# Kernel optimization log

Measured on AMD Instinct MI355X. Metric: run time of the kernel, lower is better.

Reference implementation:

```python
import jax, jax.numpy as jnp
import numpy as np

V, SMAX, D, H, L, DFF, W = 32000, 1024, 1024, 16, 2, 4096, 256
HD = D // H
EPS = 1e-6


def setup_inputs() -> dict:
    key = jax.random.key(0)
    ks = jax.random.split(key, 20)
    s = lambda k, shape, scale=0.02: jax.random.normal(k, shape, dtype=jnp.float32) * scale
    return {
        "input_ids": jax.random.randint(ks[0], (2, SMAX), 0, V, dtype=jnp.int64),
        "emb": s(ks[1], (V, D)),
        "pos": s(ks[2], (SMAX, D)),
        "norm1_w": jnp.ones((L, D), jnp.float32),
        "norm2_w": jnp.ones((L, D), jnp.float32),
        "wq": s(ks[3], (L, D, D)), "bq": jnp.zeros((L, D), jnp.float32),
        "wk": s(ks[4], (L, D, D)), "bk": jnp.zeros((L, D), jnp.float32),
        "wv": s(ks[5], (L, D, D)), "bv": jnp.zeros((L, D), jnp.float32),
        "wo": s(ks[6], (L, D, D)), "bo": jnp.zeros((L, D), jnp.float32),
        "w1": s(ks[7], (L, D, DFF)), "b1": jnp.zeros((L, DFF), jnp.float32),
        "w2": s(ks[8], (L, DFF, D)), "b2": jnp.zeros((L, D), jnp.float32),
        "normf_w": jnp.ones((D,), jnp.float32),
    }


def rms(x, w):
    return x * jax.lax.rsqrt(jnp.mean(x * x, axis=-1, keepdims=True) + EPS) * w


def reference(input_ids, emb, pos, norm1_w, norm2_w, wq, bq, wk, bk, wv, bv,
              wo, bo, w1, b1, w2, b2, normf_w):
    B, S = input_ids.shape
    x = emb[input_ids] + pos[:S]  # [B,S,D]
    # sliding-window causal mask: attend to j with 0 <= i-j < W
    i = jnp.arange(S)[:, None]
    j = jnp.arange(S)[None, :]
    mask = (j <= i) & (i - j < W)  # [S,S]
    neg = jnp.asarray(-1e9, x.dtype)
    for l in range(L):
        h = rms(x, norm1_w[l])
        q = (h @ wq[l] + bq[l]).reshape(B, S, H, HD)
        k = (h @ wk[l] + bk[l]).reshape(B, S, H, HD)
        v = (h @ wv[l] + bv[l]).reshape(B, S, H, HD)
        scores = jnp.einsum('bqhd,bkhd->bhqk', q, k) / np.sqrt(HD).astype(np.float32)
        scores = jnp.where(mask[None, None], scores, neg)
        attn = jax.nn.softmax(scores, axis=-1)
        o = jnp.einsum('bhqk,bkhd->bqhd', attn, v).reshape(B, S, D)
        x = x + (o @ wo[l] + bo[l])
        h2 = rms(x, norm2_w[l])
        x = x + (jax.nn.gelu(h2 @ w1[l] + b1[l], approximate=False) @ w2[l] + b2[l])
    x = rms(x, normf_w)
    logits = x @ emb.T  # tied lm_head
    return logits
```

## Files before the change

### kernel.cpp

```cpp
#include <hip/hip_runtime.h>
#include <hip/hip_bf16.h>
#include <cstdint>

typedef __bf16 bf16;
typedef __bf16 bf16x8 __attribute__((ext_vector_type(8)));
typedef __bf16 bf16x4 __attribute__((ext_vector_type(4)));
typedef float  f32x4  __attribute__((ext_vector_type(4)));

constexpr int V_    = 32000;
constexpr int SMAX_ = 1024;
constexpr int D_    = 1024;
constexpr int H_    = 16;
constexpr int L_    = 2;
constexpr int DFF_  = 4096;
constexpr int WIN_  = 256;
constexpr int B_    = 2;
constexpr int M_    = B_ * SMAX_;

#define SBAR0_() __builtin_amdgcn_sched_barrier(0)
#define HWBAR_() { __builtin_amdgcn_s_barrier(); SBAR0_(); }
#define LGKM0_() { asm volatile("s_waitcnt lgkmcnt(0)" ::: "memory"); SBAR0_(); }

__global__ __launch_bounds__(512, 1) void gemm256_deep(
    const bf16* __restrict__ A, const bf16* __restrict__ BT,
    float* __restrict__ outf, int Nn)
{
  constexpr int KK = 1024, NT = KK / 32;
  __shared__ __align__(16) bf16 ldsA[4 * 8192];
  __shared__ __align__(16) bf16 ldsB[4 * 8192];

  const int t = threadIdx.x, lane = t & 63, w = t >> 6;
  const int l16 = lane & 15, lh = lane >> 4;
  const int wm = w >> 2, wn = w & 3;

  const int nloc = gridDim.x >> 3;
  const int wg = (blockIdx.x & 7) * nloc + (blockIdx.x >> 3);
  const long m0 = (long)(wg & 7) * 256;
  const long n0 = (long)(wg >> 3) * 256;

  auto STG = [&](const bf16* src, long rowBase, bf16* dst, int k0) {
    #pragma unroll
    for (int j = 0; j < 2; ++j) {
      int p = j * 8192 + t * 16;
      int row = p >> 6;
      int sl = ((p >> 4) & 3) ^ (row & 3);
      const bf16* g = src + (rowBase + row) * (long)KK + k0 + sl * 8;
      __builtin_amdgcn_global_load_lds(
          (const __attribute__((address_space(1))) uint32_t*)g,
          (__attribute__((address_space(3))) uint32_t*)(dst + j * 4096 + w * 512),
          16, 0, 0);
    }
  };
  auto LDF = [&](const bf16* base, int rowb) -> bf16x8 {
    int row = rowb + l16;
    return *(const bf16x8*)(base + row * 32 + ((lh ^ (l16 & 3)) << 3));
  };

  f32x4 acc[8][4] = {};

  STG(A, m0, ldsA,          0);  STG(BT, n0, ldsB,          0);
  STG(A, m0, ldsA + 8192,  32);  STG(BT, n0, ldsB + 8192,  32);
  STG(A, m0, ldsA + 16384, 64);  STG(BT, n0, ldsB + 16384, 64);
  int kNext = 96;

  for (int i = 0; i < NT; ++i) {
    const int cur = i & 3, nb = (i + 3) & 3;
    asm volatile("s_waitcnt vmcnt(8)" ::: "memory"); SBAR0_();
    HWBAR_();
    const bf16* Ac = ldsA + cur * 8192;
    const bf16* Bc = ldsB + cur * 8192;
    bf16x8 af[8], bb[4];
    #pragma unroll
    for (int mi = 0; mi < 8; ++mi) af[mi] = LDF(Ac, wm * 128 + mi * 16);
    #pragma unroll
    for (int ni = 0; ni < 4; ++ni) bb[ni] = LDF(Bc, wn * 64 + ni * 16);
    STG(A, m0, ldsA + nb * 8192, kNext);
    STG(BT, n0, ldsB + nb * 8192, kNext);
    kNext += 32; if (kNext == KK) kNext = 0;
    LGKM0_();
    __builtin_amdgcn_s_setprio(1);
    #pragma unroll
    for (int mi = 0; mi < 8; ++mi)
      #pragma unroll
      for (int ni = 0; ni < 4; ++ni)
        acc[mi][ni] = __builtin_amdgcn_mfma_f32_16x16x32_bf16(af[mi], bb[ni], acc[mi][ni], 0, 0, 0);
    __builtin_amdgcn_s_setprio(0);
  }

  #pragma unroll
  for (int mi = 0; mi < 8; ++mi)
    #pragma unroll
    for (int ni = 0; ni < 4; ++ni)
      #pragma unroll
      for (int rr = 0; rr < 4; ++rr) {
        long row = m0 + wm * 128 + mi * 16 + lh * 4 + rr;
        long col = n0 + wn * 64 + ni * 16 + l16;
        outf[row * Nn + col] = acc[mi][ni][rr];
      }
}

template<int BM, int EPI>
__global__ __launch_bounds__(256, (BM == 128 ? 2 : 3)) void gemm_deep(
    const bf16* __restrict__ A, const bf16* __restrict__ BT,
    const float* __restrict__ bias, float* __restrict__ resid,
    bf16* __restrict__ outb, float* __restrict__ outf,
    int Nn, int Kk, int nbyMask, int nbyShift)
{
  constexpr int WR = BM / 32;
  constexpr int CA = BM / 64;
  constexpr int LPS = CA + 2;
  __shared__ __align__(16) bf16 ldsA[4 * BM * 32];
  __shared__ __align__(16) bf16 ldsB[4 * 4096];

  const int t = threadIdx.x, lane = t & 63, w = t >> 6;
  const int l16 = lane & 15, lh = lane >> 4;
  const int wm = w >> 1, wn = w & 1;

  const int nwg = gridDim.x, bid = blockIdx.x;
  const int nloc = nwg >> 3;
  const int wg = (bid & 7) * nloc + (bid >> 3);
  const long m0 = (long)(wg & nbyMask) * BM;
  const long n0 = (long)(wg >> nbyShift) * 128;

  auto STGA = [&](bf16* dst, int k0) {
    #pragma unroll
    for (int j = 0; j < CA; ++j) {
      int p = j * 4096 + t * 16;
      int row = p >> 6;
      int sl = ((p >> 4) & 3) ^ (row & 3);
      const bf16* g = A + (m0 + row) * (long)Kk + k0 + sl * 8;
      __builtin_amdgcn_global_load_lds(
          (const __attribute__((address_space(1))) uint32_t*)g,
          (__attribute__((address_space(3))) uint32_t*)(dst + j * 2048 + w * 512),
          16, 0, 0);
    }
  };
  auto STGB = [&](bf16* dst, int k0) {
    #pragma unroll
    for (int j = 0; j < 2; ++j) {
      int p = j * 4096 + t * 16;
      int row = p >> 6;
      int sl = ((p >> 4) & 3) ^ (row & 3);
      const bf16* g = BT + (n0 + row) * (long)Kk + k0 + sl * 8;
      __builtin_amdgcn_global_load_lds(
          (const __attribute__((address_space(1))) uint32_t*)g,
          (__attribute__((address_space(3))) uint32_t*)(dst + j * 2048 + w * 512),
          16, 0, 0);
    }
  };
  auto LDF = [&](const bf16* base, int rowb) -> bf16x8 {
    int row = rowb + l16;
    return *(const bf16x8*)(base + row * 32 + ((lh ^ (l16 & 3)) << 3));
  };

  f32x4 acc[WR][4] = {};

  STGA(ldsA,               0);  STGB(ldsB,        0);
  STGA(ldsA + BM * 32,    32);  STGB(ldsB + 4096, 32);
  STGA(ldsA + 2 * BM * 32, 64); STGB(ldsB + 8192, 64);
  int kNext = 96;

  const int NT = Kk >> 5;
  for (int i = 0; i < NT; ++i) {
    const int cur = i & 3, nb = (i + 3) & 3;
    if constexpr (LPS == 4) { asm volatile("s_waitcnt vmcnt(8)" ::: "memory"); }
    else                    { asm volatile("s_waitcnt vmcnt(6)" ::: "memory"); }
    SBAR0_();
    HWBAR_();
    const bf16* Ac = ldsA + cur * BM * 32;
    const bf16* Bc = ldsB + cur * 4096;
    bf16x8 af[WR], bb[4];
    #pragma unroll
    for (int mi = 0; mi < WR; ++mi) af[mi] = LDF(Ac, wm * (WR * 16) + mi * 16);
    #pragma unroll
    for (int ni = 0; ni < 4; ++ni) bb[ni] = LDF(Bc, wn * 64 + ni * 16);
    STGA(ldsA + nb * BM * 32, kNext);
    STGB(ldsB + nb * 4096, kNext);
    kNext += 32; if (kNext == Kk) kNext = 0;
    LGKM0_();
    __builtin_amdgcn_s_setprio(1);
    #pragma unroll
    for (int mi = 0; mi < WR; ++mi)
      #pragma unroll
      for (int ni = 0; ni < 4; ++ni)
        acc[mi][ni] = __builtin_amdgcn_mfma_f32_16x16x32_bf16(af[mi], bb[ni], acc[mi][ni], 0, 0, 0);
    __builtin_amdgcn_s_setprio(0);
  }

  #pragma unroll
  for (int mi = 0; mi < WR; ++mi)
    #pragma unroll
    for (int ni = 0; ni < 4; ++ni)
      #pragma unroll
      for (int rr = 0; rr < 4; ++rr) {
        long row = m0 + wm * (WR * 16) + mi * 16 + lh * 4 + rr;
        long col = n0 + wn * 64 + ni * 16 + l16;
        float v = acc[mi][ni][rr];
        if (EPI == 0) {
          outb[row * Nn + col] = (bf16)(v + bias[col]);
        } else if (EPI == 1) {
          float xx = v + bias[col];
          outb[row * Nn + col] = (bf16)(0.5f * xx * (1.0f + erff(xx * 0.70710678118654752f)));
        } else if (EPI == 2) {
          resid[row * Nn + col] += v + bias[col];
        } else {
          outf[row * Nn + col] = v;
        }
      }
}

__global__ __launch_bounds__(256) void attn_swa(
    const bf16* __restrict__ qkv, bf16* __restrict__ o)
{
  constexpr int PADK = 72;
  constexpr int PADV = 40;
  __shared__ bf16 Qs[64 * PADK];
  __shared__ bf16 Ks[32 * PADK];
  __shared__ bf16 Vt[64 * PADV];
  __shared__ bf16 Ps[4][16 * PADV];

  const int bid = blockIdx.x;
  const int qb = bid & 15;
  const int h  = (bid >> 4) & 15;
  const int b  = bid >> 8;
  const int q0 = qb * 64;
  const int t = threadIdx.x, lane = t & 63, w = t >> 6;
  const int l16 = lane & 15, lh = lane >> 4;

  #pragma unroll
  for (int i = 0; i < 2; i++) {
    int e = t + i * 256;
    int row = e >> 3, cc = e & 7;
    uint4 g = *(const uint4*)(qkv + ((long)(b * SMAX_ + q0 + row)) * 3072 + h * 64 + cc * 8);
    *(uint4*)(Qs + row * PADK + cc * 8) = g;
  }
  __syncthreads();
  bf16x8 aq[2];
  const int qrow = w * 16 + l16;
  #pragma unroll
  for (int ks = 0; ks < 2; ks++)
    aq[ks] = *(const bf16x8*)(Qs + qrow * PADK + ks * 32 + lh * 8);

  float m_run[4], l_run[4];
  f32x4 oacc[4];
  #pragma unroll
  for (int rr = 0; rr < 4; rr++) { m_run[rr] = -1e30f; l_run[rr] = 0.0f; }
  #pragma unroll
  for (int n = 0; n < 4; n++) oacc[n] = (f32x4){0.f, 0.f, 0.f, 0.f};

  const int tlo = q0 - (WIN_ - 1);
  const int jlo = (tlo <= 0) ? 0 : (tlo & ~31);
  const int iq  = q0 + w * 16 + lh * 4;

  for (int j0 = jlo; j0 < q0 + 64; j0 += 32) {
    __syncthreads();
    {
      int row = t >> 3, cc = t & 7;
      long base = ((long)(b * SMAX_ + j0 + row)) * 3072 + h * 64 + cc * 8;
      uint4 gk = *(const uint4*)(qkv + base + 1024);
      *(uint4*)(Ks + row * PADK + cc * 8) = gk;
      bf16x8 vv = *(const bf16x8*)(qkv + base + 2048);
      #pragma unroll
      for (int j = 0; j < 8; j++)
        Vt[(cc * 8 + j) * PADV + row] = vv[j];
    }
    __syncthreads();

    f32x4 s[2] = {(f32x4){0.f,0.f,0.f,0.f}, (f32x4){0.f,0.f,0.f,0.f}};
    #pragma unroll
    for (int nt = 0; nt < 2; nt++)
      #pragma unroll
      for (int ks = 0; ks < 2; ks++) {
        bf16x8 bk = *(const bf16x8*)(Ks + (nt * 16 + l16) * PADK + ks * 32 + lh * 8);
        s[nt] = __builtin_amdgcn_mfma_f32_16x16x32_bf16(aq[ks], bk, s[nt], 0, 0, 0);
      }

    float sc[2][4];
    #pragma unroll
    for (int nt = 0; nt < 2; nt++)
      #pragma unroll
      for (int rr = 0; rr < 4; rr++) {
        int i = iq + rr;
        int j = j0 + nt * 16 + l16;
        float v = s[nt][rr] * 0.125f;
        bool ok = (j <= i) && (i - j < WIN_);
        sc[nt][rr] = ok ? v : -1e30f;
      }

    float pb[2][4], alpha[4];
    #pragma unroll
    for (int rr = 0; rr < 4; rr++) {
      float mt = fmaxf(sc[0][rr], sc[1][rr]);
      #pragma unroll
      for (int off = 1; off < 16; off <<= 1) mt = fmaxf(mt, __shfl_xor(mt, off, 64));
      float mn = fmaxf(m_run[rr], mt);
      float a = __expf(m_run[rr] - mn);
      m_run[rr] = mn; alpha[rr] = a;
      float p0 = __expf(sc[0][rr] - mn);
      float p1 = __expf(sc[1][rr] - mn);
      pb[0][rr] = p0; pb[1][rr] = p1;
      float ls = p0 + p1;
      #pragma unroll
      for (int off = 1; off < 16; off <<= 1) ls += __shfl_xor(ls, off, 64);
      l_run[rr] = l_run[rr] * a + ls;
    }
    #pragma unroll
    for (int n = 0; n < 4; n++)
      #pragma unroll
      for (int rr = 0; rr < 4; rr++) oacc[n][rr] *= alpha[rr];

    #pragma unroll
    for (int rr = 0; rr < 4; rr++) {
      int prow = lh * 4 + rr;
      Ps[w][prow * PADV + l16]      = (bf16)pb[0][rr];
      Ps[w][prow * PADV + 16 + l16] = (bf16)pb[1][rr];
    }
    __syncthreads();

    bf16x8 pa = *(const bf16x8*)(&Ps[w][l16 * PADV + lh * 8]);
    #pragma unroll
    for (int n = 0; n < 4; n++) {
      bf16x8 bv = *(const bf16x8*)(Vt + (n * 16 + l16) * PADV + lh * 8);
      oacc[n] = __builtin_amdgcn_mfma_f32_16x16x32_bf16(pa, bv, oacc[n], 0, 0, 0);
    }
  }

  #pragma unroll
  for (int rr = 0; rr < 4; rr++) {
    int i = iq + rr;
    float inv = 1.0f / l_run[rr];
    #pragma unroll
    for (int n = 0; n < 4; n++)
      o[((long)(b * SMAX_ + i)) * D_ + h * 64 + n * 16 + l16] = (bf16)(oacc[n][rr] * inv);
  }
}

__global__ __launch_bounds__(256) void transpose_cvt(
    const float* __restrict__ src, bf16* __restrict__ dst,
    int Kk, int Nn, long srcL, long dstL)
{
  __shared__ float tile[32][33];
  const int tx = threadIdx.x, ty = threadIdx.y;
  const long n0 = (long)blockIdx.x * 32, k0 = (long)blockIdx.y * 32;
  src += (long)blockIdx.z * srcL;
  dst += (long)blockIdx.z * dstL;
  #pragma unroll
  for (int i = 0; i < 4; i++)
    tile[ty + i * 8][tx] = src[(k0 + ty + i * 8) * Nn + n0 + tx];
  __syncthreads();
  #pragma unroll
  for (int i = 0; i < 4; i++)
    dst[(n0 + ty + i * 8) * Kk + k0 + tx] = (bf16)tile[tx][ty + i * 8];
}

__global__ __launch_bounds__(256) void cvt_bf16(
    const float* __restrict__ src, bf16* __restrict__ dst, long n4)
{
  long i = (long)blockIdx.x * 256 + threadIdx.x;
  if (i >= n4) return;
  float4 v = ((const float4*)src)[i];
  bf16x4 o; o[0] = (bf16)v.x; o[1] = (bf16)v.y; o[2] = (bf16)v.z; o[3] = (bf16)v.w;
  ((bf16x4*)dst)[i] = o;
}

__global__ __launch_bounds__(256) void pack_bqkv(
    const float* __restrict__ bq, const float* __restrict__ bk,
    const float* __restrict__ bv, float* __restrict__ out)
{
  int i = blockIdx.x * 256 + threadIdx.x;
  if (i >= L_ * 3072) return;
  int l = i / 3072, c = i % 3072;
  float v = (c < 1024) ? bq[l * 1024 + c]
          : (c < 2048) ? bk[l * 1024 + c - 1024]
                       : bv[l * 1024 + c - 2048];
  out[i] = v;
}

__global__ __launch_bounds__(256) void embed_k(
    const int* __restrict__ ids, const float* __restrict__ emb,
    const float* __restrict__ pos, float* __restrict__ x)
{
  const int m = blockIdx.x, t = threadIdx.x;
  const int id = ids[m];
  const int s = m & (SMAX_ - 1);
  float4 e = ((const float4*)(emb + (long)id * D_))[t];
  float4 p = ((const float4*)(pos + (long)s * D_))[t];
  float4 rr; rr.x = e.x + p.x; rr.y = e.y + p.y; rr.z = e.z + p.z; rr.w = e.w + p.w;
  ((float4*)(x + (long)m * D_))[t] = rr;
}

__global__ __launch_bounds__(256) void rmsnorm_k(
    const float* __restrict__ x, const float* __restrict__ wgt,
    bf16* __restrict__ out)
{
  __shared__ float red[4];
  const int m = blockIdx.x, t = threadIdx.x;
  float4 v = ((const float4*)(x + (long)m * D_))[t];
  float ss = v.x * v.x + v.y * v.y + v.z * v.z + v.w * v.w;
  #pragma unroll
  for (int off = 1; off < 64; off <<= 1) ss += __shfl_xor(ss, off, 64);
  const int lane = t & 63, w = t >> 6;
  if (lane == 0) red[w] = ss;
  __syncthreads();
  float tot = red[0] + red[1] + red[2] + red[3];
  float rs = rsqrtf(tot * (1.0f / D_) + 1e-6f);
  float4 g = ((const float4*)wgt)[t];
  bf16x4 o;
  o[0] = (bf16)(v.x * rs * g.x); o[1] = (bf16)(v.y * rs * g.y);
  o[2] = (bf16)(v.z * rs * g.z); o[3] = (bf16)(v.w * rs * g.w);
  ((bf16x4*)(out + (long)m * D_))[t] = o;
}

extern "C" void kernel_launch(void* const* d_in, const int* in_sizes, int n_in,
                              void* d_out, int out_size, void* d_ws, size_t ws_size,
                              hipStream_t stream)
{
  const int*   ids = (const int*)d_in[0];
  const float* emb = (const float*)d_in[1];
  const float* pos = (const float*)d_in[2];
  const float* n1w = (const float*)d_in[3];
  const float* n2w = (const float*)d_in[4];
  const float* wq  = (const float*)d_in[5];
  const float* bq  = (const float*)d_in[6];
  const float* wk  = (const float*)d_in[7];
  const float* bk  = (const float*)d_in[8];
  const float* wv  = (const float*)d_in[9];
  const float* bv  = (const float*)d_in[10];
  const float* wo  = (const float*)d_in[11];
  const float* bo  = (const float*)d_in[12];
  const float* w1  = (const float*)d_in[13];
  const float* b1  = (const float*)d_in[14];
  const float* w2  = (const float*)d_in[15];
  const float* b2  = (const float*)d_in[16];
  const float* nfw = (const float*)d_in[17];

  char* p = (char*)d_ws;
  auto alloc = [&](size_t bytes) {
    char* rr = p; p += (bytes + 255) & ~(size_t)255; return rr;
  };
  bf16*  wqkv_t = (bf16*) alloc((size_t)L_ * 3 * 1024 * 1024 * 2);
  bf16*  wo_t   = (bf16*) alloc((size_t)L_ * 1024 * 1024 * 2);
  bf16*  w1_t   = (bf16*) alloc((size_t)L_ * 4096 * 1024 * 2);
  bf16*  w2_t   = (bf16*) alloc((size_t)L_ * 1024 * 4096 * 2);
  bf16*  emb_bf = (bf16*) alloc((size_t)V_ * D_ * 2);
  float* bqkv   = (float*)alloc((size_t)L_ * 3072 * 4);
  float* x      = (float*)alloc((size_t)M_ * D_ * 4);
  bf16*  hbuf   = (bf16*) alloc((size_t)M_ * D_ * 2);
  bf16*  qkv    = (bf16*) alloc((size_t)M_ * 3072 * 2);
  bf16*  obuf   = (bf16*) alloc((size_t)M_ * D_ * 2);
  bf16*  ff     = (bf16*) alloc((size_t)M_ * DFF_ * 2);

  const dim3 b32(32, 8, 1);
  transpose_cvt<<<dim3(32, 32, L_),  b32, 0, stream>>>(wq, wqkv_t,                1024, 1024, 1024 * 1024, 3 * 1024 * 1024);
  transpose_cvt<<<dim3(32, 32, L_),  b32, 0, stream>>>(wk, wqkv_t + 1024 * 1024,  1024, 1024, 1024 * 1024, 3 * 1024 * 1024);
  transpose_cvt<<<dim3(32, 32, L_),  b32, 0, stream>>>(wv, wqkv_t + 2*1024*1024,  1024, 1024, 1024 * 1024, 3 * 1024 * 1024);
  transpose_cvt<<<dim3(32, 32, L_),  b32, 0, stream>>>(wo, wo_t,                  1024, 1024, 1024 * 1024, 1024 * 1024);
  transpose_cvt<<<dim3(128, 32, L_), b32, 0, stream>>>(w1, w1_t,                  1024, 4096, 1024 * 4096, 4096 * 1024);
  transpose_cvt<<<dim3(32, 128, L_), b32, 0, stream>>>(w2, w2_t,                  4096, 1024, 4096 * 1024, 1024 * 4096);
  cvt_bf16<<<32000, 256, 0, stream>>>(emb, emb_bf, (long)V_ * D_ / 4);
  pack_bqkv<<<24, 256, 0, stream>>>(bq, bk, bv, bqkv);
  embed_k<<<M_, 256, 0, stream>>>(ids, emb, pos, x);

  for (int l = 0; l < L_; l++) {
    rmsnorm_k<<<M_, 256, 0, stream>>>(x, n1w + l * D_, hbuf);
    gemm_deep<128, 0><<<dim3(16 * 24), 256, 0, stream>>>(
        hbuf, wqkv_t + (size_t)l * 3 * 1024 * 1024, bqkv + l * 3072,
        nullptr, qkv, nullptr, 3072, 1024, 15, 4);
    attn_swa<<<B_ * H_ * (SMAX_ / 64), 256, 0, stream>>>(qkv, obuf);
    gemm_deep<64, 2><<<dim3(32 * 8), 256, 0, stream>>>(
        obuf, wo_t + (size_t)l * 1024 * 1024, bo + l * D_,
        x, nullptr, nullptr, 1024, 1024, 31, 5);
    rmsnorm_k<<<M_, 256, 0, stream>>>(x, n2w + l * D_, hbuf);
    gemm_deep<128, 1><<<dim3(16 * 32), 256, 0, stream>>>(
        hbuf, w1_t + (size_t)l * 4096 * 1024, b1 + l * DFF_,
        nullptr, ff, nullptr, 4096, 1024, 15, 4);
    gemm_deep<64, 2><<<dim3(32 * 8), 256, 0, stream>>>(
        ff, w2_t + (size_t)l * 1024 * 4096, b2 + l * D_,
        x, nullptr, nullptr, 1024, 4096, 31, 5);
  }
  rmsnorm_k<<<M_, 256, 0, stream>>>(x, nfw, hbuf);
  gemm256_deep<<<dim3(8 * (V_ / 256)), 512, 0, stream>>>(
      hbuf, emb_bf, (float*)d_out, V_);
}
```

Measured before the change: 628.4 us.

## Use 256x128 tiles with 3-stage pipeline for lm_head GEMM

Shrinks the lm_head GEMM tile from 256x256 to 256x128, doubling the number of workgroups, and cuts the LDS pipeline from four stages to three so several blocks can be resident per CU (launch bounds raised to 4). The inner loop is split into two halves of A-fragment loads with an extra barrier, which lowers register pressure. The aim is better occupancy and latency hiding on the large 2048x32000 output. In exchange, each block reuses less data per tile, fetches more A traffic in total, and pays an extra barrier per k-step.

```diff
diff --git a/kernel.cpp b/kernel.cpp
--- a/kernel.cpp
+++ b/kernel.cpp
@@ -21,13 +21,13 @@
 #define HWBAR_() { __builtin_amdgcn_s_barrier(); SBAR0_(); }
 #define LGKM0_() { asm volatile("s_waitcnt lgkmcnt(0)" ::: "memory"); SBAR0_(); }
 
-__global__ __launch_bounds__(512, 1) void gemm256_deep(
+__global__ __launch_bounds__(512, 4) void gemm256x128(
     const bf16* __restrict__ A, const bf16* __restrict__ BT,
     float* __restrict__ outf, int Nn)
 {
   constexpr int KK = 1024, NT = KK / 32;
-  __shared__ __align__(16) bf16 ldsA[4 * 8192];
-  __shared__ __align__(16) bf16 ldsB[4 * 8192];
+  __shared__ __align__(16) bf16 ldsA[3 * 8192];
+  __shared__ __align__(16) bf16 ldsB[3 * 4096];
 
   const int t = threadIdx.x, lane = t & 63, w = t >> 6;
   const int l16 = lane & 15, lh = lane >> 4;
@@ -36,65 +36,96 @@
   const int nloc = gridDim.x >> 3;
   const int wg = (blockIdx.x & 7) * nloc + (blockIdx.x >> 3);
   const long m0 = (long)(wg & 7) * 256;
-  const long n0 = (long)(wg >> 3) * 256;
-
-  auto STG = [&](const bf16* src, long rowBase, bf16* dst, int k0) {
+  const long n0 = (long)(wg >> 3) * 128;
+
+  auto STGA = [&](bf16* dst, int k0) {
     #pragma unroll
     for (int j = 0; j < 2; ++j) {
       int p = j * 8192 + t * 16;
       int row = p >> 6;
       int sl = ((p >> 4) & 3) ^ (row & 3);
-      const bf16* g = src + (rowBase + row) * (long)KK + k0 + sl * 8;
+      const bf16* g = A + (m0 + row) * (long)KK + k0 + sl * 8;
       __builtin_amdgcn_global_load_lds(
           (const __attribute__((address_space(1))) uint32_t*)g,
           (__attribute__((address_space(3))) uint32_t*)(dst + j * 4096 + w * 512),
           16, 0, 0);
     }
   };
+  auto STGB = [&](bf16* dst, int k0) {
+    int p = t * 16;
+    int row = p >> 6;
+    int sl = ((p >> 4) & 3) ^ (row & 3);
+    const bf16* g = BT + (n0 + row) * (long)KK + k0 + sl * 8;
+    __builtin_amdgcn_global_load_lds(
+        (const __attribute__((address_space(1))) uint32_t*)g,
+        (__attribute__((address_space(3))) uint32_t*)(dst + w * 512),
+        16, 0, 0);
+  };
   auto LDF = [&](const bf16* base, int rowb) -> bf16x8 {
     int row = rowb + l16;
     return *(const bf16x8*)(base + row * 32 + ((lh ^ (l16 & 3)) << 3));
   };
 
-  f32x4 acc[8][4] = {};
-
-  STG(A, m0, ldsA,          0);  STG(BT, n0, ldsB,          0);
-  STG(A, m0, ldsA + 8192,  32);  STG(BT, n0, ldsB + 8192,  32);
-  STG(A, m0, ldsA + 16384, 64);  STG(BT, n0, ldsB + 16384, 64);
-  int kNext = 96;
+  f32x4 acc[8][2] = {};
+
+  STGA(ldsA, 0);            STGB(ldsB, 0);
+  STGA(ldsA + 8192, 32);    STGB(ldsB + 4096, 32);
+  int cur = 0, stg = 2, kNext = 64;
 
   for (int i = 0; i < NT; ++i) {
-    const int cur = i & 3, nb = (i + 3) & 3;
-    asm volatile("s_waitcnt vmcnt(8)" ::: "memory"); SBAR0_();
+    asm volatile("s_waitcnt vmcnt(3)" ::: "memory"); SBAR0_();
     HWBAR_();
     const bf16* Ac = ldsA + cur * 8192;
-    const bf16* Bc = ldsB + cur * 8192;
-    bf16x8 af[8], bb[4];
-    #pragma unroll
-    for (int mi = 0; mi < 8; ++mi) af[mi] = LDF(Ac, wm * 128 + mi * 16);
-    #pragma unroll
-    for (int ni = 0; ni < 4; ++ni) bb[ni] = LDF(Bc, wn * 64 + ni * 16);
-    STG(A, m0, ldsA + nb * 8192, kNext);
-    STG(BT, n0, ldsB + nb * 8192, kNext);
+    const bf16* Bc = ldsB + cur * 4096;
+    bf16x8 bb0 = LDF(Bc, wn * 32 + 0);
+    bf16x8 bb1 = LDF(Bc, wn * 32 + 16);
+    bf16x8 a0 = LDF(Ac, wm * 128 + 0);
+    bf16x8 a1 = LDF(Ac, wm * 128 + 16);
+    bf16x8 a2 = LDF(Ac, wm * 128 + 32);
+    bf16x8 a3 = LDF(Ac, wm * 128 + 48);
+    STGA(ldsA + stg * 8192, kNext);
+    STGB(ldsB + stg * 4096, kNext);
     kNext += 32; if (kNext == KK) kNext = 0;
+    cur += 1; if (cur == 3) cur = 0;
+    stg += 1; if (stg == 3) stg = 0;
     LGKM0_();
     __builtin_amdgcn_s_setprio(1);
-    #pragma unroll
-    for (int mi = 0; mi < 8; ++mi)
-      #pragma unroll
-      for (int ni = 0; ni < 4; ++ni)
-        acc[mi][ni] = __builtin_amdgcn_mfma_f32_16x16x32_bf16(af[mi], bb[ni], acc[mi][ni], 0, 0, 0);
+    acc[0][0] = __builtin_amdgcn_mfma_f32_16x16x32_bf16(a0, bb0, acc[0][0], 0, 0, 0);
+    acc[0][1] = __builtin_amdgcn_mfma_f32_16x16x32_bf16(a0, bb1, acc[0][1], 0, 0, 0);
+    acc[1][0] = __builtin_amdgcn_mfma_f32_16x16x32_bf16(a1, bb0, acc[1][0], 0, 0, 0);
+    acc[1][1] = __builtin_amdgcn_mfma_f32_16x16x32_bf16(a1, bb1, acc[1][1], 0, 0, 0);
+    acc[2][0] = __builtin_amdgcn_mfma_f32_16x16x32_bf16(a2, bb0, acc[2][0], 0, 0, 0);
+    acc[2][1] = __builtin_amdgcn_mfma_f32_16x16x32_bf16(a2, bb1, acc[2][1], 0, 0, 0);
+    acc[3][0] = __builtin_amdgcn_mfma_f32_16x16x32_bf16(a3, bb0, acc[3][0], 0, 0, 0);
+    acc[3][1] = __builtin_amdgcn_mfma_f32_16x16x32_bf16(a3, bb1, acc[3][1], 0, 0, 0);
+    __builtin_amdgcn_s_setprio(0);
+    a0 = LDF(Ac, wm * 128 + 64);
+    a1 = LDF(Ac, wm * 128 + 80);
+    a2 = LDF(Ac, wm * 128 + 96);
+    a3 = LDF(Ac, wm * 128 + 112);
+    LGKM0_();
+    HWBAR_();
+    __builtin_amdgcn_s_setprio(1);
+    acc[4][0] = __builtin_amdgcn_mfma_f32_16x16x32_bf16(a0, bb0, acc[4][0], 0, 0, 0);
+    acc[4][1] = __builtin_amdgcn_mfma_f32_16x16x32_bf16(a0, bb1, acc[4][1], 0, 0, 0);
+    acc[5][0] = __builtin_amdgcn_mfma_f32_16x16x32_bf16(a1, bb0, acc[5][0], 0, 0, 0);
+    acc[5][1] = __builtin_amdgcn_mfma_f32_16x16x32_bf16(a1, bb1, acc[5][1], 0, 0, 0);
+    acc[6][0] = __builtin_amdgcn_mfma_f32_16x16x32_bf16(a2, bb0, acc[6][0], 0, 0, 0);
+    acc[6][1] = __builtin_amdgcn_mfma_f32_16x16x32_bf16(a2, bb1, acc[6][1], 0, 0, 0);
+    acc[7][0] = __builtin_amdgcn_mfma_f32_16x16x32_bf16(a3, bb0, acc[7][0], 0, 0, 0);
+    acc[7][1] = __builtin_amdgcn_mfma_f32_16x16x32_bf16(a3, bb1, acc[7][1], 0, 0, 0);
     __builtin_amdgcn_s_setprio(0);
   }
 
+  asm volatile("s_waitcnt vmcnt(0)" ::: "memory");
   #pragma unroll
   for (int mi = 0; mi < 8; ++mi)
     #pragma unroll
-    for (int ni = 0; ni < 4; ++ni)
+    for (int ni = 0; ni < 2; ++ni)
       #pragma unroll
       for (int rr = 0; rr < 4; ++rr) {
         long row = m0 + wm * 128 + mi * 16 + lh * 4 + rr;
-        long col = n0 + wn * 64 + ni * 16 + l16;
+        long col = n0 + wn * 32 + ni * 16 + l16;
         outf[row * Nn + col] = acc[mi][ni][rr];
       }
 }
@@ -479,6 +510,6 @@
         x, nullptr, nullptr, 1024, 4096, 31, 5);
   }
   rmsnorm_k<<<M_, 256, 0, stream>>>(x, nfw, hbuf);
-  gemm256_deep<<<dim3(8 * (V_ / 256)), 512, 0, stream>>>(
+  gemm256x128<<<dim3(8 * (V_ / 128)), 512, 0, stream>>>(
       hbuf, emb_bf, (float*)d_out, V_);
 }
```

Result: no change. 631.0 us (+0.4%).

## Load LM-head B operand directly from global into registers, LDS only for A

Applied to the files above, without the earlier changes.

Rewrites the LM-head GEMM so that only the activation tile A is staged through LDS, now double-buffered with 64-wide K steps and an 8-way XOR swizzle. The weight tile B is read straight from global memory into registers and prefetched one half-step ahead. This removes the LDS traffic and capacity used for B, and cuts the pipeline from four stages to two. The cost is B loads that are no longer shared between waves (each wave fetches its own B slice, so global and L2 traffic rises), a shallower prefetch, and latency hiding that now depends on the vmcnt waits being placed correctly.

```diff
diff --git a/kernel.cpp b/kernel.cpp
--- a/kernel.cpp
+++ b/kernel.cpp
@@ -21,13 +21,12 @@
 #define HWBAR_() { __builtin_amdgcn_s_barrier(); SBAR0_(); }
 #define LGKM0_() { asm volatile("s_waitcnt lgkmcnt(0)" ::: "memory"); SBAR0_(); }
 
-__global__ __launch_bounds__(512, 1) void gemm256_deep(
+__global__ __launch_bounds__(512) void gemm_lm_bdirect(
     const bf16* __restrict__ A, const bf16* __restrict__ BT,
     float* __restrict__ outf, int Nn)
 {
-  constexpr int KK = 1024, NT = KK / 32;
-  __shared__ __align__(16) bf16 ldsA[4 * 8192];
-  __shared__ __align__(16) bf16 ldsB[4 * 8192];
+  constexpr int KK = 1024, NT = 16;
+  __shared__ __align__(16) bf16 ldsA[2][16384];
 
   const int t = threadIdx.x, lane = t & 63, w = t >> 6;
   const int l16 = lane & 15, lh = lane >> 4;
@@ -38,55 +37,73 @@
   const long m0 = (long)(wg & 7) * 256;
   const long n0 = (long)(wg >> 3) * 256;
 
-  auto STG = [&](const bf16* src, long rowBase, bf16* dst, int k0) {
-    #pragma unroll
-    for (int j = 0; j < 2; ++j) {
-      int p = j * 8192 + t * 16;
-      int row = p >> 6;
-      int sl = ((p >> 4) & 3) ^ (row & 3);
-      const bf16* g = src + (rowBase + row) * (long)KK + k0 + sl * 8;
+  auto STGA = [&](int c, int k0) {
+    #pragma unroll
+    for (int q = 0; q < 4; ++q) {
+      int row = q * 64 + (t >> 3);
+      int sl  = (t & 7) ^ (row & 7);
+      const bf16* g = A + (m0 + row) * (long)KK + k0 + sl * 8;
       __builtin_amdgcn_global_load_lds(
           (const __attribute__((address_space(1))) uint32_t*)g,
-          (__attribute__((address_space(3))) uint32_t*)(dst + j * 4096 + w * 512),
+          (__attribute__((address_space(3))) uint32_t*)(&ldsA[c][q * 4096 + t * 8]),
           16, 0, 0);
     }
   };
-  auto LDF = [&](const bf16* base, int rowb) -> bf16x8 {
-    int row = rowb + l16;
-    return *(const bf16x8*)(base + row * 32 + ((lh ^ (l16 & 3)) << 3));
+  auto LDA = [&](int c, int mi, int ks) -> bf16x8 {
+    int row = wm * 128 + mi * 16 + l16;
+    int sl  = (ks * 4 + lh) ^ (row & 7);
+    return *(const bf16x8*)(&ldsA[c][row * 64 + sl * 8]);
+  };
+  auto BADDR = [&](int ni, int kk) -> const bf16* {
+    return BT + (n0 + wn * 64 + ni * 16 + l16) * (long)KK + kk + lh * 8;
   };
 
   f32x4 acc[8][4] = {};
-
-  STG(A, m0, ldsA,          0);  STG(BT, n0, ldsB,          0);
-  STG(A, m0, ldsA + 8192,  32);  STG(BT, n0, ldsB + 8192,  32);
-  STG(A, m0, ldsA + 16384, 64);  STG(BT, n0, ldsB + 16384, 64);
-  int kNext = 96;
-
-  for (int i = 0; i < NT; ++i) {
-    const int cur = i & 3, nb = (i + 3) & 3;
+  bf16x8 a[8], b0[4], b1[4];
+
+  STGA(0, 0);
+  SBAR0_();
+  #pragma unroll
+  for (int ni = 0; ni < 4; ++ni) b0[ni] = *(const bf16x8*)BADDR(ni, 0);
+
+  for (int j = 0; j < NT; ++j) {
+    const int c = j & 1;
+    const int kc = j * 64;
+    const int kn = (kc + 64) & (KK - 1);
+    asm volatile("s_waitcnt vmcnt(4)" ::: "memory"); SBAR0_();
+    HWBAR_();
+    #pragma unroll
+    for (int mi = 0; mi < 8; ++mi) a[mi] = LDA(c, mi, 0);
+    #pragma unroll
+    for (int ni = 0; ni < 4; ++ni) b1[ni] = *(const bf16x8*)BADDR(ni, kc + 32);
+    LGKM0_();
+    asm volatile("s_waitcnt vmcnt(4)" ::: "memory"); SBAR0_();
+    __builtin_amdgcn_s_setprio(1);
+    #pragma unroll
+    for (int mi = 0; mi < 8; ++mi)
+      #pragma unroll
+      for (int ni = 0; ni < 4; ++ni)
+        acc[mi][ni] = __builtin_amdgcn_mfma_f32_16x16x32_bf16(a[mi], b0[ni], acc[mi][ni], 0, 0, 0);
+    __builtin_amdgcn_s_setprio(0);
+    SBAR0_();
+    #pragma unroll
+    for (int mi = 0; mi < 8; ++mi) a[mi] = LDA(c, mi, 1);
+    STGA(c ^ 1, kn);
+    SBAR0_();
+    #pragma unroll
+    for (int ni = 0; ni < 4; ++ni) b0[ni] = *(const bf16x8*)BADDR(ni, kn);
+    LGKM0_();
     asm volatile("s_waitcnt vmcnt(8)" ::: "memory"); SBAR0_();
-    HWBAR_();
-    const bf16* Ac = ldsA + cur * 8192;
-    const bf16* Bc = ldsB + cur * 8192;
-    bf16x8 af[8], bb[4];
-    #pragma unroll
-    for (int mi = 0; mi < 8; ++mi) af[mi] = LDF(Ac, wm * 128 + mi * 16);
-    #pragma unroll
-    for (int ni = 0; ni < 4; ++ni) bb[ni] = LDF(Bc, wn * 64 + ni * 16);
-    STG(A, m0, ldsA + nb * 8192, kNext);
-    STG(BT, n0, ldsB + nb * 8192, kNext);
-    kNext += 32; if (kNext == KK) kNext = 0;
-    LGKM0_();
     __builtin_amdgcn_s_setprio(1);
     #pragma unroll
     for (int mi = 0; mi < 8; ++mi)
       #pragma unroll
       for (int ni = 0; ni < 4; ++ni)
-        acc[mi][ni] = __builtin_amdgcn_mfma_f32_16x16x32_bf16(af[mi], bb[ni], acc[mi][ni], 0, 0, 0);
+        acc[mi][ni] = __builtin_amdgcn_mfma_f32_16x16x32_bf16(a[mi], b1[ni], acc[mi][ni], 0, 0, 0);
     __builtin_amdgcn_s_setprio(0);
   }
 
+  asm volatile("s_waitcnt vmcnt(0) lgkmcnt(0)" ::: "memory");
   #pragma unroll
   for (int mi = 0; mi < 8; ++mi)
     #pragma unroll
@@ -479,6 +496,6 @@
         x, nullptr, nullptr, 1024, 4096, 31, 5);
   }
   rmsnorm_k<<<M_, 256, 0, stream>>>(x, nfw, hbuf);
-  gemm256_deep<<<dim3(8 * (V_ / 256)), 512, 0, stream>>>(
+  gemm_lm_bdirect<<<dim3(8 * (V_ / 256)), 512, 0, stream>>>(
       hbuf, emb_bf, (float*)d_out, V_);
 }
```

New measurement: 650.1 us. 1.03x slower.
